# Optimization experiments

Measured on AMD Instinct MI355X. Metric: run time of the kernel, lower is better.

The kernel has to match this reference:

```python
import jax, jax.numpy as jnp
import numpy as np

B, DIM, X, Y = 2, 256, 48, 48
HEADS, DIM_HEAD = 8, 64
DIM_INNER = HEADS * DIM_HEAD
MASK_SELF_VALUE = -100.0
EPS = 1e-12


def setup_inputs() -> dict:
    key = jax.random.key(0)
    k0, k1, k2, k3, k4 = jax.random.split(key, 5)
    return {
        "fmap": jax.random.normal(k0, (B, DIM, X, Y), dtype=jnp.float32),
        "gamma": jnp.ones((DIM,), dtype=jnp.float32),
        "w_qk": jax.random.normal(k1, (DIM_INNER, DIM), dtype=jnp.float32) * 0.02,
        "w_v": jax.random.normal(k2, (DIM_INNER, DIM), dtype=jnp.float32) * 0.02,
        "null_kv": jax.random.normal(k3, (2, HEADS, DIM_HEAD), dtype=jnp.float32),
        "w_out": jax.random.normal(k4, (DIM, DIM_INNER), dtype=jnp.float32) * 0.02,
    }


def _safe_sqrt(d2):
    # matches torch.cdist subgradient: zero grad at zero distance
    pos = d2 > 0
    return jnp.where(pos, jnp.sqrt(jnp.where(pos, d2, 1.0)), 0.0)


def reference(fmap, gamma, w_qk, w_v, null_kv, w_out):
    b, c, x, y = fmap.shape
    h, dh = HEADS, DIM_HEAD
    n = x * y
    scale = dh ** -0.5

    # ChannelRMSNorm: L2-normalize over channel dim, * sqrt(dim) * gamma
    l2 = jnp.sqrt(jnp.sum(fmap * fmap, axis=1, keepdims=True))
    normed = fmap / jnp.maximum(l2, EPS) * jnp.sqrt(jnp.float32(c)) * gamma[None, :, None, None]

    flat = normed.reshape(b, c, n)                       # b c n
    qk = jnp.einsum('oc,bcn->bon', w_qk, flat)           # b (h d) n
    v = jnp.einsum('oc,bcn->bon', w_v, flat)
    qk = qk.reshape(b, h, dh, n).transpose(0, 1, 3, 2)   # b h n d
    v = v.reshape(b, h, dh, n).transpose(0, 1, 3, 2)

    nk = jnp.broadcast_to(null_kv[0][None, :, None, :], (b, h, 1, dh))
    nv = jnp.broadcast_to(null_kv[1][None, :, None, :], (b, h, 1, dh))
    q = qk
    k = jnp.concatenate([nk, qk], axis=2)                # b h (n+1) d
    vv = jnp.concatenate([nv, v], axis=2)

    # -cdist(q, k, p=2) * scale via squared-distance expansion
    q2 = jnp.sum(q * q, axis=-1)[..., :, None]           # b h n 1
    k2 = jnp.sum(k * k, axis=-1)[..., None, :]           # b h 1 n+1
    cross = jnp.einsum('bhid,bhjd->bhij', q, k)          # b h n n+1
    d2 = jnp.maximum(q2 + k2 - 2.0 * cross, 0.0)
    sim = -_safe_sqrt(d2) * scale

    # mask self: eye(n) left-padded by one (null token never masked)
    self_mask = jnp.eye(n, n + 1, k=1, dtype=bool)
    sim = jnp.where(self_mask, MASK_SELF_VALUE, sim)

    attn = jax.nn.softmax(sim, axis=-1)
    out = jnp.einsum('bhij,bhjd->bhid', attn, vv)        # b h n d
    out = out.transpose(0, 1, 3, 2).reshape(b, h * dh, x, y)
    return jnp.einsum('oc,bcxy->boxy', w_out, out)
```

## Files before the change

kernel.cpp:

```cpp
#include <hip/hip_runtime.h>
#include <math.h>

#define NPOS 2304
#define CC   256
#define DI   512
#define NT   36
#define SCALE 0.125f
#define MASKV -100.0f
#define NEGSL2E (-0.18033688011112042f)

typedef __attribute__((ext_vector_type(8))) short bf16x8;
typedef __attribute__((ext_vector_type(4))) float f32x4;
typedef unsigned short u16;
typedef unsigned int u32;

__device__ inline u16 f2bf(float f) {
    union { float f; unsigned int u; } v; v.f = f;
    return (u16)((v.u + 0x7fffu + ((v.u >> 16) & 1u)) >> 16);
}
__device__ inline float bf2f(u16 h) { return __uint_as_float(((u32)h) << 16); }

__device__ inline bf16x8 ld_x8(const u16* p) {
    union { bf16x8 v; uint2 d[2]; } u;
    u.d[0] = *(const uint2*)(p + 0);
    u.d[1] = *(const uint2*)(p + 4);
    return u.v;
}

__device__ __forceinline__ void gl16(const u16* g, u16* l) {
    __builtin_amdgcn_global_load_lds(
        (const __attribute__((address_space(1))) void*)g,
        (__attribute__((address_space(3))) void*)l, 16, 0, 0);
}

__global__ __launch_bounds__(256) void k_prep(const float* __restrict__ wqk,
                                              const float* __restrict__ wv,
                                              const float* __restrict__ wout,
                                              u16* __restrict__ wqkh,
                                              u16* __restrict__ wvh,
                                              u16* __restrict__ wo_hi,
                                              u16* __restrict__ wo_lo) {
    const int blk = blockIdx.x;
    const int t = threadIdx.x;
    if (blk < 128) {
        const int k = blk * 256 + t;
        const float4 v = ((const float4*)wqk)[k];
        ushort4 h4;
        h4.x = f2bf(v.x); h4.y = f2bf(v.y); h4.z = f2bf(v.z); h4.w = f2bf(v.w);
        ((ushort4*)wqkh)[k] = h4;
    } else if (blk < 256) {
        const int k = (blk - 128) * 256 + t;
        const float4 v = ((const float4*)wv)[k];
        ushort4 h4;
        h4.x = f2bf(v.x); h4.y = f2bf(v.y); h4.z = f2bf(v.z); h4.w = f2bf(v.w);
        ((ushort4*)wvh)[k] = h4;
    } else {
        const int k = (blk - 256) * 256 + t;
        const float4 v = ((const float4*)wout)[k];
        ushort4 h4, l4;
        h4.x = f2bf(v.x); l4.x = f2bf(v.x - bf2f(h4.x));
        h4.y = f2bf(v.y); l4.y = f2bf(v.y - bf2f(h4.y));
        h4.z = f2bf(v.z); l4.z = f2bf(v.z - bf2f(h4.z));
        h4.w = f2bf(v.w); l4.w = f2bf(v.w - bf2f(h4.w));
        ((ushort4*)wo_hi)[k] = h4;
        ((ushort4*)wo_lo)[k] = l4;
    }
}

__global__ __launch_bounds__(256) void k_proj(const float* __restrict__ fmap,
                                              const float* __restrict__ gamma,
                                              const u16* __restrict__ wqkh,
                                              const u16* __restrict__ wvh,
                                              const float* __restrict__ null_kv,
                                              u16* __restrict__ qkh,
                                              u16* __restrict__ vt,
                                              float* __restrict__ sq,
                                              float* __restrict__ ndot,
                                              float* __restrict__ nk2b) {
    const int blk = blockIdx.x;
    const int xcd = blk & 7;
    const int r   = blk >> 3;
    const int bh  = xcd * 2 + (r & 1);
    const int b   = bh >> 3;
    const int oy  = bh & 7;
    const int n0  = (r >> 1) * 64;

    const int t  = threadIdx.x;
    const int w = t >> 6, lane = t & 63, mcol = lane & 15, quad = lane >> 4;
    const int tx = t & 63, ty = t >> 6;

    __shared__ u16 X[64][260];
    __shared__ float red[4][64];
    __shared__ float inv_s[64];
    __shared__ float gs[256];
    __shared__ float sqp[4][64], ndp[4][64];
    u16 (*Tt)[68] = (u16(*)[68])X;

    gs[t] = gamma[t];
    const float* fb = fmap + (size_t)b * CC * NPOS;
    float v64[64];
#pragma unroll
    for (int i = 0; i < 64; ++i)
        v64[i] = fb[(ty * 64 + i) * NPOS + n0 + tx];
    float s = 0.0f;
#pragma unroll
    for (int i = 0; i < 64; ++i) s += v64[i] * v64[i];
    red[ty][tx] = s;
    __syncthreads();
    if (t < 64) {
        const float tt = red[0][t] + red[1][t] + red[2][t] + red[3][t];
        inv_s[t] = 16.0f / fmaxf(sqrtf(tt), 1e-12f);
    }
    __syncthreads();
    const float iv = inv_s[tx];
#pragma unroll
    for (int i = 0; i < 64; i += 2) {
        const int c = ty * 64 + i;
        const float v0 = v64[i] * iv * gs[c];
        const float v1 = v64[i + 1] * iv * gs[c + 1];
        *(u32*)&X[tx][c] = (u32)f2bf(v0) | ((u32)f2bf(v1) << 16);
    }
    if (blk == 0 && t < 8) {
        float s2 = 0.0f;
#pragma unroll 8
        for (int d = 0; d < 64; ++d) { const float x = null_kv[t * 64 + d]; s2 += x * x; }
        nk2b[t] = s2;
    }
    __syncthreads();

    const size_t wroff = (size_t)(oy * 64 + w * 16 + mcol) * 256 + quad * 8;
    const u16* wrq = wqkh + wroff;
    const u16* wrv = wvh + wroff;

    f32x4 cq[4], cv[4];
#pragma unroll
    for (int nf = 0; nf < 4; ++nf) {
        cq[nf] = (f32x4){0.f, 0.f, 0.f, 0.f};
        cv[nf] = (f32x4){0.f, 0.f, 0.f, 0.f};
    }
#pragma unroll
    for (int kc = 0; kc < 8; ++kc) {
        const bf16x8 aq = *(const bf16x8*)&wrq[kc * 32];
        const bf16x8 av = *(const bf16x8*)&wrv[kc * 32];
        bf16x8 xB[4];
#pragma unroll
        for (int nf = 0; nf < 4; ++nf)
            xB[nf] = ld_x8(&X[nf * 16 + mcol][kc * 32 + quad * 8]);
#pragma unroll
        for (int nf = 0; nf < 4; ++nf) {
            cq[nf] = __builtin_amdgcn_mfma_f32_16x16x32_bf16(aq, xB[nf], cq[nf], 0, 0, 0);
            cv[nf] = __builtin_amdgcn_mfma_f32_16x16x32_bf16(av, xB[nf], cv[nf], 0, 0, 0);
        }
    }
    __syncthreads();

    {
        const int h = oy;
        const float4 nk4 = *(const float4*)&null_kv[h * 64 + w * 16 + quad * 4];
        float sv[4], nd[4];
#pragma unroll
        for (int nf = 0; nf < 4; ++nf) {
            sv[nf] = cq[nf][0] * cq[nf][0] + cq[nf][1] * cq[nf][1] + cq[nf][2] * cq[nf][2] + cq[nf][3] * cq[nf][3];
            nd[nf] = cq[nf][0] * nk4.x + cq[nf][1] * nk4.y + cq[nf][2] * nk4.z + cq[nf][3] * nk4.w;
        }
#pragma unroll
        for (int mk = 16; mk <= 32; mk <<= 1)
#pragma unroll
            for (int nf = 0; nf < 4; ++nf) {
                sv[nf] += __shfl_xor(sv[nf], mk);
                nd[nf] += __shfl_xor(nd[nf], mk);
            }
        if (quad == 0) {
#pragma unroll
            for (int nf = 0; nf < 4; ++nf) {
                sqp[w][nf * 16 + mcol] = sv[nf];
                ndp[w][nf * 16 + mcol] = nd[nf];
            }
        }
#pragma unroll
        for (int nf = 0; nf < 4; ++nf) {
            ushort4 r4;
            r4.x = f2bf(cq[nf][0]); r4.y = f2bf(cq[nf][1]);
            r4.z = f2bf(cq[nf][2]); r4.w = f2bf(cq[nf][3]);
            *(ushort4*)&Tt[nf * 16 + mcol][w * 16 + quad * 4] = r4;
        }
        __syncthreads();
        {
            const int n = t >> 2, ds = (t & 3) * 16;
            const uint2 r0 = *(const uint2*)&Tt[n][ds + 0];
            const uint2 r1 = *(const uint2*)&Tt[n][ds + 4];
            const uint2 r2 = *(const uint2*)&Tt[n][ds + 8];
            const uint2 r3 = *(const uint2*)&Tt[n][ds + 12];
            u16* dst = qkh + (((size_t)bh) * NPOS + n0 + n) * 64 + ds;
            *(uint4*)&dst[0] = make_uint4(r0.x, r0.y, r1.x, r1.y);
            *(uint4*)&dst[8] = make_uint4(r2.x, r2.y, r3.x, r3.y);
        }
        if (t < 64) {
            sq  [((size_t)bh) * NPOS + n0 + t] = sqp[0][t] + sqp[1][t] + sqp[2][t] + sqp[3][t];
            ndot[((size_t)bh) * NPOS + n0 + t] = ndp[0][t] + ndp[1][t] + ndp[2][t] + ndp[3][t];
        }
    }
    __syncthreads();

    {
#pragma unroll
        for (int nf = 0; nf < 4; ++nf)
#pragma unroll
            for (int rr = 0; rr < 4; ++rr)
                Tt[w * 16 + quad * 4 + rr][nf * 16 + mcol] = f2bf(cv[nf][rr]);
        __syncthreads();
        {
            const int d = t >> 2, ks = t & 3;
            const uint2 a0 = *(const uint2*)&Tt[d][ks * 16 + 0];
            const uint2 a1 = *(const uint2*)&Tt[d][ks * 16 + 4];
            const uint2 a2 = *(const uint2*)&Tt[d][ks * 16 + 8];
            const uint2 a3 = *(const uint2*)&Tt[d][ks * 16 + 12];
            u16* vdst = vt + (size_t)bh * (72 * 64 * 32);
            const int kb = (n0 >> 5) + (ks >> 1);
            u16* p = &vdst[((size_t)kb * 64 + d) * 32 + (ks & 1) * 16];
            *(uint4*)&p[0] = make_uint4(a0.x, a0.y, a1.x, a1.y);
            *(uint4*)&p[8] = make_uint4(a2.x, a2.y, a3.x, a3.y);
        }
    }
}

template <int KS>
__global__ __launch_bounds__(256) void k_attn(const u16* __restrict__ qkh,
                                              const u16* __restrict__ vt,
                                              const float* __restrict__ null_kv,
                                              const float* __restrict__ nk2b,
                                              const float* __restrict__ sq,
                                              const float* __restrict__ ndot,
                                              u16* __restrict__ ih,
                                              u16* __restrict__ il,
                                              float* __restrict__ pO,
                                              float* __restrict__ pL) {
    const int blk = blockIdx.x;
    const int xcd = blk & 7;
    const int j = blk >> 3;
    const int bh = xcd * 2 + (j & 1);
    const int r2 = j >> 1;
    const int qt = (KS == 2) ? (r2 >> 1) : r2;
    const int kh = (KS == 2) ? (r2 & 1) : 0;
    const int q0 = qt * 64;
    const int b = bh >> 3, h = bh & 7;
    const int t = threadIdx.x;
    const int wave = t >> 6, lane = t & 63;
    const int mcol = lane & 15, quad = lane >> 4;

    const int kt0 = kh * 18;
    const int NTL = (KS == 2) ? 18 : 36;

    __shared__ __align__(16) u16 sm[20992];
    u16* Kls = sm;
    u16* Vls = sm + 8192;
    u16 (*Pt)[72] = (u16(*)[72])(sm + 16384 + wave * 1152);

    const u16* qbase = qkh + (size_t)bh * NPOS * 64;
    const u16* vbase = vt + (size_t)bh * (72 * 64 * 32);
    const float* sqb = sq + (size_t)bh * NPOS;

    const int q16 = q0 + wave * 16;
    const bf16x8 bq00 = *(const bf16x8*)&qbase[(q16 + mcol) * 64 + quad * 8];
    const bf16x8 bq01 = *(const bf16x8*)&qbase[(q16 + mcol) * 64 + 32 + quad * 8];
    const float q2 = sqb[q16 + mcol];
    const int ktm = q16 >> 6;
    const int nbm = (q16 >> 4) & 3;

    const int kbase0 = (wave * 16 + 0) * 64;
    const int kbase1 = (wave * 16 + 8) * 64;
    const int ksrc0 = (wave * 16 + 0 + (lane >> 3)) * 64 + ((lane & 7) ^ (lane >> 3)) * 8;
    const int ksrc1 = (wave * 16 + 8 + (lane >> 3)) * 64 + ((lane & 7) ^ (lane >> 3)) * 8;
    const int vldsb = wave * 512;
    const int vsrc = (wave * 16 + (lane >> 2)) * 32 + ((lane & 3) ^ ((lane >> 3) & 3)) * 8;

    const int m7 = mcol & 7;
    const int mv = (mcol >> 1) & 3;

    {
        const u16* kg = qbase + (size_t)kt0 * 4096;
        const u16* vg = vbase + (size_t)kt0 * 4096;
        gl16(kg + ksrc0, Kls + kbase0);
        gl16(kg + ksrc1, Kls + kbase1);
        gl16(vg + vsrc,        Vls + vldsb);
        gl16(vg + 2048 + vsrc, Vls + 2048 + vldsb);
    }

    const bf16x8 ones = {0x3F80, 0x3F80, 0x3F80, 0x3F80, 0x3F80, 0x3F80, 0x3F80, 0x3F80};

    f32x4 oacc[4];
#pragma unroll
    for (int nb = 0; nb < 4; ++nb) oacc[nb] = (f32x4){0.f, 0.f, 0.f, 0.f};
    f32x4 lsum = (f32x4){0.f, 0.f, 0.f, 0.f};

    int p = 0;
#pragma unroll 1
    for (int i = 0; i < NTL; ++i) {
        const int kt = kt0 + i;
        __syncthreads();
        float4 k2q[4];
#pragma unroll
        for (int nb = 0; nb < 4; ++nb)
            k2q[nb] = *(const float4*)&sqb[kt * 64 + nb * 16 + quad * 4];
        if (i + 1 < NTL) {
            const u16* kg = qbase + (size_t)(kt + 1) * 4096;
            const u16* vg = vbase + (size_t)(kt + 1) * 4096;
            const int bb = (p ^ 1) * 4096;
            gl16(kg + ksrc0, Kls + bb + kbase0);
            gl16(kg + ksrc1, Kls + bb + kbase1);
            gl16(vg + vsrc,        Vls + bb + vldsb);
            gl16(vg + 2048 + vsrc, Vls + bb + 2048 + vldsb);
        }

        const u16* Kb = Kls + p * 4096;
        const u16* Vb = Vls + p * 4096;

        bf16x8 bk[4][2];
#pragma unroll
        for (int nb = 0; nb < 4; ++nb) {
            const int rr = (nb * 16 + mcol) * 64;
            bk[nb][0] = *(const bf16x8*)&Kb[rr + ((quad ^ m7)) * 8];
            bk[nb][1] = *(const bf16x8*)&Kb[rr + (((4 + quad) ^ m7)) * 8];
        }

        f32x4 c[4];
#pragma unroll
        for (int nb = 0; nb < 4; ++nb) {
            c[nb] = (f32x4){0.f, 0.f, 0.f, 0.f};
            c[nb] = __builtin_amdgcn_mfma_f32_16x16x32_bf16(bk[nb][0], bq00, c[nb], 0, 0, 0);
            c[nb] = __builtin_amdgcn_mfma_f32_16x16x32_bf16(bk[nb][1], bq01, c[nb], 0, 0, 0);
        }

        bf16x8 bv[4][2];
#pragma unroll
        for (int nb = 0; nb < 4; ++nb) {
            const int rr = (nb * 16 + mcol) * 32 + ((quad ^ mv)) * 8;
            bv[nb][0] = *(const bf16x8*)&Vb[rr];
            bv[nb][1] = *(const bf16x8*)&Vb[2048 + rr];
        }

#pragma unroll
        for (int nb = 0; nb < 4; ++nb) {
            float e[4];
#pragma unroll
            for (int r = 0; r < 4; ++r) {
                const float pre = q2 + ((const float*)&k2q[nb])[r];
                const float d2 = fmaxf(__builtin_fmaf(c[nb][r], -2.0f, pre), 0.0f);
                e[r] = __builtin_amdgcn_exp2f(NEGSL2E * __builtin_amdgcn_sqrtf(d2));
            }
            if (kt == ktm && nb == nbm) {
#pragma unroll
                for (int r = 0; r < 4; ++r)
                    if (quad * 4 + r == mcol) e[r] = 0.0f;
            }
            const u32 p01 = __builtin_amdgcn_perm(__float_as_uint(e[1]), __float_as_uint(e[0]), 0x07060302u);
            const u32 p23 = __builtin_amdgcn_perm(__float_as_uint(e[3]), __float_as_uint(e[2]), 0x07060302u);
            *(uint2*)&Pt[mcol][nb * 16 + quad * 4] = make_uint2(p01, p23);
        }

        const bf16x8 bp00 = *(const bf16x8*)&Pt[mcol][quad * 8];
        const bf16x8 bp01 = *(const bf16x8*)&Pt[mcol][32 + quad * 8];

#pragma unroll
        for (int nb = 0; nb < 4; ++nb) {
            oacc[nb] = __builtin_amdgcn_mfma_f32_16x16x32_bf16(bv[nb][0], bp00, oacc[nb], 0, 0, 0);
            oacc[nb] = __builtin_amdgcn_mfma_f32_16x16x32_bf16(bv[nb][1], bp01, oacc[nb], 0, 0, 0);
        }
        lsum = __builtin_amdgcn_mfma_f32_16x16x32_bf16(ones, bp00, lsum, 0, 0, 0);
        lsum = __builtin_amdgcn_mfma_f32_16x16x32_bf16(ones, bp01, lsum, 0, 0, 0);

        p ^= 1;
    }

    __syncthreads();

    float* Ofin = (float*)sm + wave * (16 * 68);
#pragma unroll
    for (int nb = 0; nb < 4; ++nb)
        *(f32x4*)&Ofin[mcol * 68 + nb * 16 + quad * 4] = oacc[nb];
    if (quad == 0) Ofin[mcol * 68 + 64] = lsum[0];

    {
        const int q = lane >> 2;
        const int d0 = (lane & 3) * 16;
        const float4 a0 = *(const float4*)&Ofin[q * 68 + d0 + 0];
        const float4 a1 = *(const float4*)&Ofin[q * 68 + d0 + 4];
        const float4 a2 = *(const float4*)&Ofin[q * 68 + d0 + 8];
        const float4 a3 = *(const float4*)&Ofin[q * 68 + d0 + 12];
        const float l = Ofin[q * 68 + 64];
        const int qg = q16 + q;

        if (KS == 2) {
            float* dst = pO + (size_t)kh * 2359296 + ((size_t)bh * NPOS + qg) * 64 + d0;
            *(float4*)&dst[0]  = a0;
            *(float4*)&dst[4]  = a1;
            *(float4*)&dst[8]  = a2;
            *(float4*)&dst[12] = a3;
            if ((lane & 3) == 0)
                pL[(size_t)kh * 36864 + (size_t)bh * NPOS + qg] = l;
        } else {
            const float q2v = sqb[qg];
            const float nd = ndot[(size_t)bh * NPOS + qg];
            const float nk2 = nk2b[h];
            const float d2n = fmaxf(q2v + nk2 - 2.0f * nd, 0.0f);
            const float beta = __expf(-sqrtf(d2n) * SCALE);
            const float ilv = 1.0f / (l + beta);

            const float* nvp = &null_kv[DI + h * 64 + d0];
            const float4 nv0 = *(const float4*)&nvp[0];
            const float4 nv1 = *(const float4*)&nvp[4];
            const float4 nv2 = *(const float4*)&nvp[8];
            const float4 nv3 = *(const float4*)&nvp[12];

            const size_t ob = ((size_t)b * NPOS + qg) * DI + h * 64 + d0;
            float vv[16];
            vv[0]  = (a0.x + beta * nv0.x) * ilv; vv[1]  = (a0.y + beta * nv0.y) * ilv;
            vv[2]  = (a0.z + beta * nv0.z) * ilv; vv[3]  = (a0.w + beta * nv0.w) * ilv;
            vv[4]  = (a1.x + beta * nv1.x) * ilv; vv[5]  = (a1.y + beta * nv1.y) * ilv;
            vv[6]  = (a1.z + beta * nv1.z) * ilv; vv[7]  = (a1.w + beta * nv1.w) * ilv;
            vv[8]  = (a2.x + beta * nv2.x) * ilv; vv[9]  = (a2.y + beta * nv2.y) * ilv;
            vv[10] = (a2.z + beta * nv2.z) * ilv; vv[11] = (a2.w + beta * nv2.w) * ilv;
            vv[12] = (a3.x + beta * nv3.x) * ilv; vv[13] = (a3.y + beta * nv3.y) * ilv;
            vv[14] = (a3.z + beta * nv3.z) * ilv; vv[15] = (a3.w + beta * nv3.w) * ilv;
#pragma unroll
            for (int g = 0; g < 4; ++g) {
                ushort4 hi4, lo4;
                hi4.x = f2bf(vv[g * 4 + 0]); lo4.x = f2bf(vv[g * 4 + 0] - bf2f(hi4.x));
                hi4.y = f2bf(vv[g * 4 + 1]); lo4.y = f2bf(vv[g * 4 + 1] - bf2f(hi4.y));
                hi4.z = f2bf(vv[g * 4 + 2]); lo4.z = f2bf(vv[g * 4 + 2] - bf2f(hi4.z));
                hi4.w = f2bf(vv[g * 4 + 3]); lo4.w = f2bf(vv[g * 4 + 3] - bf2f(hi4.w));
                *(ushort4*)&ih[ob + g * 4] = hi4;
                *(ushort4*)&il[ob + g * 4] = lo4;
            }
        }
    }
}

__global__ __launch_bounds__(256) void k_merge(const float* __restrict__ pO,
                                               const float* __restrict__ pL,
                                               const float* __restrict__ null_kv,
                                               const float* __restrict__ nk2b,
                                               const float* __restrict__ sq,
                                               const float* __restrict__ ndot,
                                               u16* __restrict__ ih,
                                               u16* __restrict__ il) {
    const int gid = blockIdx.x * 256 + (int)threadIdx.x;
    const int d0 = (gid & 3) * 16;
    const int t2 = gid >> 2;
    const int bh = t2 / NPOS;
    const int qg = t2 - bh * NPOS;
    const int b = bh >> 3, h = bh & 7;

    const size_t o0 = ((size_t)bh * NPOS + qg) * 64 + d0;
    const size_t o1 = o0 + 2359296;
    const float4 a0 = *(const float4*)&pO[o0 + 0];
    const float4 a1 = *(const float4*)&pO[o0 + 4];
    const float4 a2 = *(const float4*)&pO[o0 + 8];
    const float4 a3 = *(const float4*)&pO[o0 + 12];
    const float4 c0 = *(const float4*)&pO[o1 + 0];
    const float4 c1 = *(const float4*)&pO[o1 + 4];
    const float4 c2 = *(const float4*)&pO[o1 + 8];
    const float4 c3 = *(const float4*)&pO[o1 + 12];
    const float l = pL[(size_t)bh * NPOS + qg] + pL[36864 + (size_t)bh * NPOS + qg];

    const float q2v = sq[(size_t)bh * NPOS + qg];
    const float nd = ndot[(size_t)bh * NPOS + qg];
    const float nk2 = nk2b[h];
    const float d2n = fmaxf(q2v + nk2 - 2.0f * nd, 0.0f);
    const float beta = __expf(-sqrtf(d2n) * SCALE);
    const float ilv = 1.0f / (l + beta);

    const float* nvp = &null_kv[DI + h * 64 + d0];
    const float4 nv0 = *(const float4*)&nvp[0];
    const float4 nv1 = *(const float4*)&nvp[4];
    const float4 nv2 = *(const float4*)&nvp[8];
    const float4 nv3 = *(const float4*)&nvp[12];

    float vv[16];
    vv[0]  = (a0.x + c0.x + beta * nv0.x) * ilv; vv[1]  = (a0.y + c0.y + beta * nv0.y) * ilv;
    vv[2]  = (a0.z + c0.z + beta * nv0.z) * ilv; vv[3]  = (a0.w + c0.w + beta * nv0.w) * ilv;
    vv[4]  = (a1.x + c1.x + beta * nv1.x) * ilv; vv[5]  = (a1.y + c1.y + beta * nv1.y) * ilv;
    vv[6]  = (a1.z + c1.z + beta * nv1.z) * ilv; vv[7]  = (a1.w + c1.w + beta * nv1.w) * ilv;
    vv[8]  = (a2.x + c2.x + beta * nv2.x) * ilv; vv[9]  = (a2.y + c2.y + beta * nv2.y) * ilv;
    vv[10] = (a2.z + c2.z + beta * nv2.z) * ilv; vv[11] = (a2.w + c2.w + beta * nv2.w) * ilv;
    vv[12] = (a3.x + c3.x + beta * nv3.x) * ilv; vv[13] = (a3.y + c3.y + beta * nv3.y) * ilv;
    vv[14] = (a3.z + c3.z + beta * nv3.z) * ilv; vv[15] = (a3.w + c3.w + beta * nv3.w) * ilv;

    const size_t ob = ((size_t)b * NPOS + qg) * DI + h * 64 + d0;
#pragma unroll
    for (int g = 0; g < 4; ++g) {
        ushort4 hi4, lo4;
        hi4.x = f2bf(vv[g * 4 + 0]); lo4.x = f2bf(vv[g * 4 + 0] - bf2f(hi4.x));
        hi4.y = f2bf(vv[g * 4 + 1]); lo4.y = f2bf(vv[g * 4 + 1] - bf2f(hi4.y));
        hi4.z = f2bf(vv[g * 4 + 2]); lo4.z = f2bf(vv[g * 4 + 2] - bf2f(hi4.z));
        hi4.w = f2bf(vv[g * 4 + 3]); lo4.w = f2bf(vv[g * 4 + 3] - bf2f(hi4.w));
        *(ushort4*)&ih[ob + g * 4] = hi4;
        *(ushort4*)&il[ob + g * 4] = lo4;
    }
}

__global__ __launch_bounds__(256) void k_out(const u16* __restrict__ wo_hi,
                                             const u16* __restrict__ wo_lo,
                                             const u16* __restrict__ ih,
                                             const u16* __restrict__ il,
                                             float* __restrict__ out) {
    const int j0 = blockIdx.x * 32;
    const int c0 = blockIdx.y * 64;
    const int b  = blockIdx.z;
    const int t  = threadIdx.x;
    const int w = t >> 6, lane = t & 63, mcol = lane & 15, quad = lane >> 4;

    __shared__ __align__(16) u16 Bst[2][2][32][64];

    const u16* ah = wo_hi + (size_t)(c0 + w * 16 + mcol) * 512 + quad * 8;
    const u16* al = wo_lo + (size_t)(c0 + w * 16 + mcol) * 512 + quad * 8;

    const size_t bsrc_row = (size_t)b * NPOS + j0 + w * 8 + (lane >> 3);
    const int bsg = ((lane & 7) ^ (lane >> 3)) * 8;
    const u16* bsrc_h = ih + bsrc_row * 512 + bsg;
    const u16* bsrc_l = il + bsrc_row * 512 + bsg;
    u16* bdst_h = &Bst[0][0][w * 8][0];
    u16* bdst_l = &Bst[0][1][w * 8][0];

    gl16(bsrc_h, bdst_h);
    gl16(bsrc_l, bdst_l);

    f32x4 c[2];
    c[0] = (f32x4){0.f, 0.f, 0.f, 0.f};
    c[1] = (f32x4){0.f, 0.f, 0.f, 0.f};

    int p = 0;
#pragma unroll 1
    for (int ph = 0; ph < 8; ++ph) {
        __syncthreads();
        if (ph + 1 < 8) {
            const int ko = (ph + 1) * 64;
            gl16(bsrc_h + ko, bdst_h + (p ^ 1) * 4096);
            gl16(bsrc_l + ko, bdst_l + (p ^ 1) * 4096);
        }
        const u16* Bb = &Bst[p][0][0][0];
#pragma unroll
        for (int sub = 0; sub < 2; ++sub) {
            const int kc = ph * 2 + sub;
            const bf16x8 A  = *(const bf16x8*)&ah[kc * 32];
            const bf16x8 Al = *(const bf16x8*)&al[kc * 32];
#pragma unroll
            for (int nf = 0; nf < 2; ++nf) {
                const int r = nf * 16 + mcol;
                const int g = (sub * 4 + quad) ^ (r & 7);
                const bf16x8 Bh = *(const bf16x8*)&Bb[r * 64 + g * 8];
                const bf16x8 Bl = *(const bf16x8*)&Bb[2048 + r * 64 + g * 8];
                c[nf] = __builtin_amdgcn_mfma_f32_16x16x32_bf16(A,  Bh, c[nf], 0, 0, 0);
                c[nf] = __builtin_amdgcn_mfma_f32_16x16x32_bf16(A,  Bl, c[nf], 0, 0, 0);
                c[nf] = __builtin_amdgcn_mfma_f32_16x16x32_bf16(Al, Bh, c[nf], 0, 0, 0);
            }
        }
        p ^= 1;
    }
    float* ob = out + ((size_t)b * CC + c0 + w * 16) * NPOS + j0;
#pragma unroll
    for (int nf = 0; nf < 2; ++nf)
#pragma unroll
        for (int r = 0; r < 4; ++r)
            ob[(size_t)(quad * 4 + r) * NPOS + nf * 16 + mcol] = c[nf][r];
}

extern "C" void kernel_launch(void* const* d_in, const int* in_sizes, int n_in,
                              void* d_out, int out_size, void* d_ws, size_t ws_size,
                              hipStream_t stream) {
    const float* fmap    = (const float*)d_in[0];
    const float* gamma   = (const float*)d_in[1];
    const float* w_qk    = (const float*)d_in[2];
    const float* w_v     = (const float*)d_in[3];
    const float* null_kv = (const float*)d_in[4];
    const float* w_out   = (const float*)d_in[5];
    float* out = (float*)d_out;

    u16* ws16 = (u16*)d_ws;
    u16* qkh    = ws16;
    u16* vtb    = qkh + 2359296;
    u16* in_hi  = vtb + 2359296;
    u16* in_lo  = in_hi + 2359296;
    u16* wo_hi  = in_lo + 2359296;
    u16* wo_lo  = wo_hi + 131072;
    u16* wqkh   = wo_lo + 131072;
    u16* wvh    = wqkh + 131072;
    float* sqbuf = (float*)(wvh + 131072);
    float* ndbuf = sqbuf + 36864;
    float* nk2b  = ndbuf + 36864;
    float* pOws  = nk2b + 8;
    float* pLws  = pOws + 4718592;
    const size_t need_split = (size_t)((char*)(pLws + 73728) - (char*)d_ws);

    hipLaunchKernelGGL(k_prep, dim3(384),       dim3(256), 0, stream,
                       w_qk, w_v, w_out, wqkh, wvh, wo_hi, wo_lo);
    hipLaunchKernelGGL(k_proj, dim3(576),       dim3(256), 0, stream,
                       fmap, gamma, wqkh, wvh, null_kv, qkh, vtb, sqbuf, ndbuf, nk2b);
    if (ws_size >= need_split) {
        hipLaunchKernelGGL(HIP_KERNEL_NAME(k_attn<2>), dim3(1152), dim3(256), 0, stream,
                           qkh, vtb, null_kv, nk2b, sqbuf, ndbuf, in_hi, in_lo, pOws, pLws);
        hipLaunchKernelGGL(k_merge, dim3(576),  dim3(256), 0, stream,
                           pOws, pLws, null_kv, nk2b, sqbuf, ndbuf, in_hi, in_lo);
    } else {
        hipLaunchKernelGGL(HIP_KERNEL_NAME(k_attn<1>), dim3(576), dim3(256), 0, stream,
                           qkh, vtb, null_kv, nk2b, sqbuf, ndbuf, in_hi, in_lo, pOws, pLws);
    }
    hipLaunchKernelGGL(k_out,  dim3(72, 4, 2),  dim3(256), 0, stream,
                       wo_hi, wo_lo, in_hi, in_lo, out);
}
```

Before: 155.5 us.

## Hoist RMS-norm into prep kernel, load normalized bf16 tiles via swizzled LDS DMA

```diff
diff --git a/kernel.cpp b/kernel.cpp
--- a/kernel.cpp
+++ b/kernel.cpp
@@ -33,42 +33,89 @@
         (__attribute__((address_space(3))) void*)l, 16, 0, 0);
 }
 
-__global__ __launch_bounds__(256) void k_prep(const float* __restrict__ wqk,
-                                              const float* __restrict__ wv,
-                                              const float* __restrict__ wout,
-                                              u16* __restrict__ wqkh,
-                                              u16* __restrict__ wvh,
-                                              u16* __restrict__ wo_hi,
-                                              u16* __restrict__ wo_lo) {
+__global__ __launch_bounds__(256) void k_pre(const float* __restrict__ fmap,
+                                             const float* __restrict__ gamma,
+                                             const float* __restrict__ wqk,
+                                             const float* __restrict__ wv,
+                                             const float* __restrict__ wout,
+                                             u16* __restrict__ xn,
+                                             u16* __restrict__ wqkh,
+                                             u16* __restrict__ wvh,
+                                             u16* __restrict__ wo_hi,
+                                             u16* __restrict__ wo_lo) {
     const int blk = blockIdx.x;
     const int t = threadIdx.x;
-    if (blk < 128) {
-        const int k = blk * 256 + t;
-        const float4 v = ((const float4*)wqk)[k];
-        ushort4 h4;
-        h4.x = f2bf(v.x); h4.y = f2bf(v.y); h4.z = f2bf(v.z); h4.w = f2bf(v.w);
-        ((ushort4*)wqkh)[k] = h4;
-    } else if (blk < 256) {
-        const int k = (blk - 128) * 256 + t;
-        const float4 v = ((const float4*)wv)[k];
-        ushort4 h4;
-        h4.x = f2bf(v.x); h4.y = f2bf(v.y); h4.z = f2bf(v.z); h4.w = f2bf(v.w);
-        ((ushort4*)wvh)[k] = h4;
-    } else {
-        const int k = (blk - 256) * 256 + t;
-        const float4 v = ((const float4*)wout)[k];
-        ushort4 h4, l4;
-        h4.x = f2bf(v.x); l4.x = f2bf(v.x - bf2f(h4.x));
-        h4.y = f2bf(v.y); l4.y = f2bf(v.y - bf2f(h4.y));
-        h4.z = f2bf(v.z); l4.z = f2bf(v.z - bf2f(h4.z));
-        h4.w = f2bf(v.w); l4.w = f2bf(v.w - bf2f(h4.w));
-        ((ushort4*)wo_hi)[k] = h4;
-        ((ushort4*)wo_lo)[k] = l4;
-    }
-}
-
-__global__ __launch_bounds__(256) void k_proj(const float* __restrict__ fmap,
-                                              const float* __restrict__ gamma,
+    if (blk >= 72) {
+        const int idx = blk - 72;
+        if (idx < 128) {
+            const int k = idx * 256 + t;
+            const float4 v = ((const float4*)wqk)[k];
+            ushort4 h4;
+            h4.x = f2bf(v.x); h4.y = f2bf(v.y); h4.z = f2bf(v.z); h4.w = f2bf(v.w);
+            ((ushort4*)wqkh)[k] = h4;
+        } else if (idx < 256) {
+            const int k = (idx - 128) * 256 + t;
+            const float4 v = ((const float4*)wv)[k];
+            ushort4 h4;
+            h4.x = f2bf(v.x); h4.y = f2bf(v.y); h4.z = f2bf(v.z); h4.w = f2bf(v.w);
+            ((ushort4*)wvh)[k] = h4;
+        } else {
+            const int k = (idx - 256) * 256 + t;
+            const float4 v = ((const float4*)wout)[k];
+            ushort4 h4, l4;
+            h4.x = f2bf(v.x); l4.x = f2bf(v.x - bf2f(h4.x));
+            h4.y = f2bf(v.y); l4.y = f2bf(v.y - bf2f(h4.y));
+            h4.z = f2bf(v.z); l4.z = f2bf(v.z - bf2f(h4.z));
+            h4.w = f2bf(v.w); l4.w = f2bf(v.w - bf2f(h4.w));
+            ((ushort4*)wo_hi)[k] = h4;
+            ((ushort4*)wo_lo)[k] = l4;
+        }
+        return;
+    }
+    const int b = blk & 1, n0 = (blk >> 1) * 64;
+    const int tx = t & 63, ty = t >> 6;
+    __shared__ u16 X[64][260];
+    __shared__ float red[4][64];
+    __shared__ float inv_s[64];
+    __shared__ float gs[256];
+
+    gs[t] = gamma[t];
+    const float* fb = fmap + (size_t)b * CC * NPOS;
+    float v64[64];
+#pragma unroll
+    for (int i = 0; i < 64; ++i)
+        v64[i] = fb[(ty * 64 + i) * NPOS + n0 + tx];
+    float s = 0.0f;
+#pragma unroll
+    for (int i = 0; i < 64; ++i) s += v64[i] * v64[i];
+    red[ty][tx] = s;
+    __syncthreads();
+    if (t < 64) {
+        const float tt = red[0][t] + red[1][t] + red[2][t] + red[3][t];
+        inv_s[t] = 16.0f / fmaxf(sqrtf(tt), 1e-12f);
+    }
+    __syncthreads();
+    const float iv = inv_s[tx];
+#pragma unroll
+    for (int i = 0; i < 64; i += 2) {
+        const int c = ty * 64 + i;
+        const float v0 = v64[i] * iv * gs[c];
+        const float v1 = v64[i + 1] * iv * gs[c + 1];
+        *(u32*)&X[tx][c] = (u32)f2bf(v0) | ((u32)f2bf(v1) << 16);
+    }
+    __syncthreads();
+    u16* xb = xn + ((size_t)b * NPOS + n0) * 256;
+#pragma unroll
+    for (int k = 0; k < 8; ++k) {
+        const int gran = k * 256 + t;
+        const int row = gran >> 5, colg = gran & 31;
+        const uint2 lo = *(const uint2*)&X[row][colg * 8];
+        const uint2 hi = *(const uint2*)&X[row][colg * 8 + 4];
+        *(uint4*)&xb[(size_t)gran * 8] = make_uint4(lo.x, lo.y, hi.x, hi.y);
+    }
+}
+
+__global__ __launch_bounds__(256) void k_proj(const u16* __restrict__ xn,
                                               const u16* __restrict__ wqkh,
                                               const u16* __restrict__ wvh,
                                               const float* __restrict__ null_kv,
@@ -87,38 +134,21 @@
 
     const int t  = threadIdx.x;
     const int w = t >> 6, lane = t & 63, mcol = lane & 15, quad = lane >> 4;
-    const int tx = t & 63, ty = t >> 6;
-
-    __shared__ u16 X[64][260];
-    __shared__ float red[4][64];
-    __shared__ float inv_s[64];
-    __shared__ float gs[256];
+
+    __shared__ __align__(16) u16 Xl[16384];
     __shared__ float sqp[4][64], ndp[4][64];
-    u16 (*Tt)[68] = (u16(*)[68])X;
-
-    gs[t] = gamma[t];
-    const float* fb = fmap + (size_t)b * CC * NPOS;
-    float v64[64];
-#pragma unroll
-    for (int i = 0; i < 64; ++i)
-        v64[i] = fb[(ty * 64 + i) * NPOS + n0 + tx];
-    float s = 0.0f;
-#pragma unroll
-    for (int i = 0; i < 64; ++i) s += v64[i] * v64[i];
-    red[ty][tx] = s;
-    __syncthreads();
-    if (t < 64) {
-        const float tt = red[0][t] + red[1][t] + red[2][t] + red[3][t];
-        inv_s[t] = 16.0f / fmaxf(sqrtf(tt), 1e-12f);
-    }
-    __syncthreads();
-    const float iv = inv_s[tx];
-#pragma unroll
-    for (int i = 0; i < 64; i += 2) {
-        const int c = ty * 64 + i;
-        const float v0 = v64[i] * iv * gs[c];
-        const float v1 = v64[i + 1] * iv * gs[c + 1];
-        *(u32*)&X[tx][c] = (u32)f2bf(v0) | ((u32)f2bf(v1) << 16);
+    u16 (*Tt)[68] = (u16(*)[68])Xl;
+
+    const u16* xg = xn + ((size_t)b * NPOS + n0) * 256;
+    {
+        const int r01 = lane >> 5;
+        const int jg = lane & 31;
+#pragma unroll
+        for (int rr = 0; rr < 8; ++rr) {
+            const int row = rr * 8 + w * 2 + r01;
+            gl16(xg + (size_t)row * 256 + (size_t)((jg ^ (row & 7)) * 8),
+                 Xl + (rr * 8 + w * 2) * 256);
+        }
     }
     if (blk == 0 && t < 8) {
         float s2 = 0.0f;
@@ -144,8 +174,11 @@
         const bf16x8 av = *(const bf16x8*)&wrv[kc * 32];
         bf16x8 xB[4];
 #pragma unroll
-        for (int nf = 0; nf < 4; ++nf)
-            xB[nf] = ld_x8(&X[nf * 16 + mcol][kc * 32 + quad * 8]);
+        for (int nf = 0; nf < 4; ++nf) {
+            const int row = nf * 16 + mcol;
+            const int g = (kc * 4 + quad) ^ (row & 7);
+            xB[nf] = *(const bf16x8*)&Xl[row * 256 + g * 8];
+        }
 #pragma unroll
         for (int nf = 0; nf < 4; ++nf) {
             cq[nf] = __builtin_amdgcn_mfma_f32_16x16x32_bf16(aq, xB[nf], cq[nf], 0, 0, 0);
@@ -585,17 +618,18 @@
     u16* wo_lo  = wo_hi + 131072;
     u16* wqkh   = wo_lo + 131072;
     u16* wvh    = wqkh + 131072;
-    float* sqbuf = (float*)(wvh + 131072);
+    u16* xnb    = wvh + 131072;
+    float* sqbuf = (float*)(xnb + 1179648);
     float* ndbuf = sqbuf + 36864;
     float* nk2b  = ndbuf + 36864;
     float* pOws  = nk2b + 8;
     float* pLws  = pOws + 4718592;
     const size_t need_split = (size_t)((char*)(pLws + 73728) - (char*)d_ws);
 
-    hipLaunchKernelGGL(k_prep, dim3(384),       dim3(256), 0, stream,
-                       w_qk, w_v, w_out, wqkh, wvh, wo_hi, wo_lo);
+    hipLaunchKernelGGL(k_pre,  dim3(456),       dim3(256), 0, stream,
+                       fmap, gamma, w_qk, w_v, w_out, xnb, wqkh, wvh, wo_hi, wo_lo);
     hipLaunchKernelGGL(k_proj, dim3(576),       dim3(256), 0, stream,
-                       fmap, gamma, wqkh, wvh, null_kv, qkh, vtb, sqbuf, ndbuf, nk2b);
+                       xnb, wqkh, wvh, null_kv, qkh, vtb, sqbuf, ndbuf, nk2b);
     if (ws_size >= need_split) {
         hipLaunchKernelGGL(HIP_KERNEL_NAME(k_attn<2>), dim3(1152), dim3(256), 0, stream,
                            qkh, vtb, null_kv, nk2b, sqbuf, ndbuf, in_hi, in_lo, pOws, pLws);
```

New measurement: 156.3 us. No clear change (+0.5%).
